# Kernel tuning notes

Measured on AMD Instinct MI355X. Metric: run time of the kernel, lower is better.

Reference implementation:

```python
import jax, jax.numpy as jnp
import numpy as np
import math

MAX_T = 1000

def _timestep_emb(t, emb_dim):
    half = emb_dim // 2
    freqs = jnp.exp(jnp.arange(half, dtype=jnp.float32) * -(math.log(MAX_T) / (half - 1)))
    e = t.astype(jnp.float32)[:, None] * freqs[None, :]
    return jnp.concatenate([jnp.sin(e), jnp.cos(e)], axis=1)  # [bs, emb_dim]


def setup_inputs() -> dict:
    key = jax.random.key(0)
    ks = jax.random.split(key, 12)
    BS, N, D, H = 16, 1024, 128, 8  # batch, nodes(=in_channels), out_dim(=d), heads
    w = lambda k, shape: jax.random.normal(k, shape, dtype=jnp.float32) * 0.05
    return {
        "A_t": jax.random.normal(ks[0], (BS, N, N), dtype=jnp.float32),
        "F_c": jax.random.normal(ks[1], (BS, N, D), dtype=jnp.float32),
        "t": jax.random.randint(ks[2], (BS,), 0, MAX_T),
        "Wq": w(ks[3], (D, D * H)), "bq": jnp.zeros((D * H,), jnp.float32),
        "Wk": w(ks[4], (D, D * H)), "bk": jnp.zeros((D * H,), jnp.float32),
        "Wv": w(ks[5], (D, D * H)), "bv": jnp.zeros((D * H,), jnp.float32),
        "Wo": w(ks[6], (D * H, D)), "bo": jnp.zeros((D,), jnp.float32),
        "Wg": jnp.eye(D, dtype=jnp.float32),  # GCN weight, eye init
    }


def reference(A_t, F_c, t, Wq, bq, Wk, bk, Wv, bv, Wo, bo, Wg):
    BS, N, D = F_c.shape
    H = Wq.shape[1] // D
    # timestep embedding, emb_dim = in_channels = N
    t_emb = _timestep_emb(t, N)                       # [bs, N]
    c = F_c + t_emb[:, :, None]                       # [bs, N, D]
    # naive multi-head self-attention with per-head dim = out_dim
    q = (c @ Wq + bq).reshape(BS, N, H, D).transpose(0, 2, 1, 3)
    k = (c @ Wk + bk).reshape(BS, N, H, D).transpose(0, 2, 1, 3)
    v = (c @ Wv + bv).reshape(BS, N, H, D).transpose(0, 2, 1, 3)
    scores = jnp.einsum('bhnd,bhmd->bhnm', q, k) / math.sqrt(D)
    a = jax.nn.softmax(scores, axis=-1)
    ctx = jnp.einsum('bhnm,bhmd->bhnd', a, v)
    ctx = ctx.transpose(0, 2, 1, 3).reshape(BS, N, H * D)
    h = ctx @ Wo + bo                                 # [bs, N, D]
    # GCN: relu(A @ (h @ W))
    feat = jax.nn.relu(A_t @ (h @ Wg))                # [bs, N, D]
    # Corr: row-normalize (unbiased std, matching torch.std) then bmm
    mu = feat.mean(axis=-1, keepdims=True)
    std = jnp.std(feat, axis=-1, ddof=1, keepdims=True)
    norm = (feat - mu) / (std + 1e-8)
    return jnp.einsum('bnd,bmd->bnm', norm, norm) / feat.shape[-1]
```

## Files before the change

### kernel.cpp

```cpp
#include <hip/hip_runtime.h>
#include <math.h>

#define NN 1024
#define DD 128
#define HH 8

typedef __attribute__((ext_vector_type(8))) short short8;
typedef __attribute__((ext_vector_type(4))) float f32x4;

__device__ inline unsigned short f2bf(float x) {
    union { float f; unsigned u; } v; v.f = x;
    return (unsigned short)((v.u + 0x7FFF + ((v.u >> 16) & 1)) >> 16);
}
__device__ inline unsigned pack2(float a, float b) {
    return (unsigned)f2bf(a) | ((unsigned)f2bf(b) << 16);
}

__global__ __launch_bounds__(256) void k_prep_w(
    const float* __restrict__ Wq, const float* __restrict__ Wk, const float* __restrict__ Wv,
    const float* __restrict__ Wo, const float* __restrict__ Wg,
    unsigned short* WqT, unsigned short* WkT, unsigned short* WvT,
    unsigned short* WoT, unsigned short* WgT) {
    int id = blockIdx.x;
    const float* src; unsigned short* dst; int R, C, ti;
    if (id < 128)      { src = Wq; dst = WqT; R = 128;  C = 1024; ti = id; }
    else if (id < 256) { src = Wk; dst = WkT; R = 128;  C = 1024; ti = id - 128; }
    else if (id < 384) { src = Wv; dst = WvT; R = 128;  C = 1024; ti = id - 256; }
    else if (id < 512) { src = Wo; dst = WoT; R = 1024; C = 128;  ti = id - 384; }
    else               { src = Wg; dst = WgT; R = 128;  C = 128;  ti = id - 512; }
    int tc = C >> 5;
    int r0 = (ti / tc) << 5, c0 = (ti % tc) << 5;
    __shared__ float T[32][33];
    int tid = threadIdx.x;
    int r = tid >> 3, c4 = (tid & 7) << 2;
    float4 v = *(const float4*)&src[(size_t)(r0 + r) * C + c0 + c4];
    T[r][c4] = v.x; T[r][c4 + 1] = v.y; T[r][c4 + 2] = v.z; T[r][c4 + 3] = v.w;
    __syncthreads();
    int c = tid >> 3, r4 = (tid & 7) << 2;
    uint2 o;
    o.x = pack2(T[r4][c], T[r4 + 1][c]);
    o.y = pack2(T[r4 + 2][c], T[r4 + 3][c]);
    *(uint2*)&dst[(size_t)(c0 + c) * R + r0 + r4] = o;
}

__global__ __launch_bounds__(256) void k_embed(const float* __restrict__ F_c,
                                               const int* __restrict__ t,
                                               unsigned short* __restrict__ cb) {
    int gi = blockIdx.x * 256 + threadIdx.x;
    int row = gi >> 4, ch = gi & 15;
    int b = row >> 10, n = row & 1023;
    float tv = (float)t[b];
    int j = n & 511;
    float e = tv * expf(-(float)j * 0.013518112092919054f);
    float emb = (n < 512) ? sinf(e) : cosf(e);
    const float* src = F_c + (size_t)row * 128 + ch * 8;
    float4 a = *(const float4*)src;
    float4 c4 = *(const float4*)(src + 4);
    uint4 o;
    o.x = pack2(a.x + emb, a.y + emb);  o.y = pack2(a.z + emb, a.w + emb);
    o.z = pack2(c4.x + emb, c4.y + emb); o.w = pack2(c4.z + emb, c4.w + emb);
    *(uint4*)&cb[(size_t)row * 128 + ch * 8] = o;
}

__global__ __launch_bounds__(256) void k_proj(const unsigned short* __restrict__ Ain,
                                              const unsigned short* __restrict__ WT,
                                              const float* __restrict__ bias,
                                              unsigned short* __restrict__ Out,
                                              float scale, int mode, int bh_mul) {
    __shared__ __align__(16) unsigned short sm[2 * 128 * 136];
    unsigned short* CT  = sm;
    unsigned short* WTs = sm + 128 * 136;
    int tid = threadIdx.x;
    int m0 = blockIdx.x * 128;
    int head = blockIdx.y;
    int w = tid >> 6, lane = tid & 63, n16 = lane & 15, quad = lane >> 4;
#pragma unroll
    for (int p = 0; p < 8; ++p) {
        int idx = tid + p * 256;
        int r = idx >> 4, ch = idx & 15;
        *(uint4*)&CT[r * 136 + ch * 8]  = *(const uint4*)&Ain[(size_t)(m0 + r) * 128 + ch * 8];
        *(uint4*)&WTs[r * 136 + ch * 8] = *(const uint4*)&WT[(size_t)(head * 128 + r) * 128 + ch * 8];
    }
    __syncthreads();
    int wr = (w >> 1) * 64, wc = (w & 1) * 64;
    f32x4 acc[4][4];
#pragma unroll
    for (int i = 0; i < 4; i++)
#pragma unroll
        for (int j = 0; j < 4; j++) acc[i][j] = (f32x4){0.f, 0.f, 0.f, 0.f};
#pragma unroll
    for (int kk = 0; kk < 4; ++kk) {
        short8 af[4], bf[4];
#pragma unroll
        for (int rb = 0; rb < 4; ++rb)
            af[rb] = *(const short8*)&CT[(wr + rb * 16 + n16) * 136 + kk * 32 + quad * 8];
#pragma unroll
        for (int cb = 0; cb < 4; ++cb)
            bf[cb] = *(const short8*)&WTs[(wc + cb * 16 + n16) * 136 + kk * 32 + quad * 8];
#pragma unroll
        for (int rb = 0; rb < 4; ++rb)
#pragma unroll
            for (int cb = 0; cb < 4; ++cb)
                acc[rb][cb] = __builtin_amdgcn_mfma_f32_16x16x32_bf16(af[rb], bf[cb], acc[rb][cb], 0, 0, 0);
    }
    __syncthreads();
#pragma unroll
    for (int rb = 0; rb < 4; ++rb)
#pragma unroll
        for (int cb = 0; cb < 4; ++cb) {
            int colb = wc + cb * 16 + n16;
            float bs = bias ? bias[head * 128 + colb] : 0.f;
#pragma unroll
            for (int reg = 0; reg < 4; ++reg) {
                int rowb = wr + rb * 16 + quad * 4 + reg;
                unsigned short val = f2bf((acc[rb][cb][reg] + bs) * scale);
                if (mode == 0) CT[rowb * 136 + colb] = val;
                else           CT[colb * 136 + rowb] = val;
            }
        }
    __syncthreads();
    int b = m0 >> 10, n0 = m0 & 1023;
    size_t base = (size_t)(b * bh_mul + head) * 131072;
    if (mode == 0) {
#pragma unroll
        for (int p = 0; p < 8; ++p) {
            int idx = tid + p * 256;
            int r = idx >> 4, ch = idx & 15;
            *(uint4*)&Out[base + (size_t)(n0 + r) * 128 + ch * 8] = *(const uint4*)&CT[r * 136 + ch * 8];
        }
    } else {
#pragma unroll
        for (int p = 0; p < 8; ++p) {
            int idx = tid + p * 256;
            int r = idx >> 4, ch = idx & 15;
            *(uint4*)&Out[base + (size_t)r * 1024 + n0 + ch * 8] = *(const uint4*)&CT[r * 136 + ch * 8];
        }
    }
}

__global__ __launch_bounds__(256, 2) void k_attn2(const unsigned short* __restrict__ qbuf,
                                                  const unsigned short* __restrict__ kbuf,
                                                  const unsigned short* __restrict__ vtb,
                                                  unsigned short* __restrict__ ctxb) {
    __shared__ __align__(16) unsigned short sm[17920];
    unsigned short* Ks = sm;
    unsigned short* Vt = sm + 8704;

    const int tid = threadIdx.x;
    const int w = tid >> 6, lane = tid & 63;
    const int n16 = lane & 15, quad = lane >> 4;
    const int g = blockIdx.x;
    const int bh = g & 127, tileq = g >> 7;

    const unsigned short* Qp = qbuf + (size_t)bh * 131072 + (size_t)tileq * 16384;
    const unsigned short* Kp = kbuf + (size_t)bh * 131072;
    const unsigned short* Vp = vtb + (size_t)bh * 131072;

    short8 qf[2][4];
#pragma unroll
    for (int qb2 = 0; qb2 < 2; ++qb2)
#pragma unroll
        for (int dc = 0; dc < 4; ++dc)
            qf[qb2][dc] = *(const short8*)&Qp[(size_t)(w * 32 + qb2 * 16 + n16) * 128 + dc * 32 + quad * 8];

    float mrun[2] = {-1e30f, -1e30f};
    float lrun[2] = {0.f, 0.f};
    f32x4 O[2][8];
#pragma unroll
    for (int qb2 = 0; qb2 < 2; ++qb2)
#pragma unroll
        for (int dc = 0; dc < 8; ++dc) O[qb2][dc] = (f32x4){0.f, 0.f, 0.f, 0.f};

    const int vr0 = tid >> 3;
    const int k0 = (tid & 7) * 8;
    const int slotA = ((k0 >> 5) << 5) | (((k0 >> 2) & 3) << 3) | (((k0 >> 4) & 1) << 2);

    uint4 kreg[4], vreg[4];
#pragma unroll
    for (int p = 0; p < 4; ++p) {
        int idx = tid + p * 256;
        int r = idx >> 4, ch = idx & 15;
        kreg[p] = *(const uint4*)&Kp[(size_t)r * 128 + ch * 8];
        vreg[p] = *(const uint4*)&Vp[(size_t)(vr0 + p * 32) * 1024 + k0];
    }

    for (int kt = 0; kt < 16; ++kt) {
#pragma unroll
        for (int p = 0; p < 4; ++p) {
            int idx = tid + p * 256;
            int r = idx >> 4, ch = idx & 15;
            *(uint4*)&Ks[r * 136 + ch * 8] = kreg[p];
        }
#pragma unroll
        for (int p = 0; p < 4; ++p) {
            int r = vr0 + p * 32;
            *(uint2*)&Vt[r * 72 + slotA]     = make_uint2(vreg[p].x, vreg[p].y);
            *(uint2*)&Vt[r * 72 + slotA + 8] = make_uint2(vreg[p].z, vreg[p].w);
        }
        __syncthreads();

        if (kt < 15) {
#pragma unroll
            for (int p = 0; p < 4; ++p) {
                int idx = tid + p * 256;
                int r = idx >> 4, ch = idx & 15;
                kreg[p] = *(const uint4*)&Kp[(size_t)((kt + 1) * 64 + r) * 128 + ch * 8];
                vreg[p] = *(const uint4*)&Vp[(size_t)(vr0 + p * 32) * 1024 + (kt + 1) * 64 + k0];
            }
        }

        f32x4 S[2][4];
#pragma unroll
        for (int qb2 = 0; qb2 < 2; ++qb2)
#pragma unroll
            for (int kb = 0; kb < 4; ++kb) S[qb2][kb] = (f32x4){0.f, 0.f, 0.f, 0.f};
        __builtin_amdgcn_s_setprio(1);
#pragma unroll
        for (int kb = 0; kb < 4; ++kb)
#pragma unroll
            for (int dc = 0; dc < 4; ++dc) {
                short8 kf = *(const short8*)&Ks[(kb * 16 + n16) * 136 + dc * 32 + quad * 8];
                S[0][kb] = __builtin_amdgcn_mfma_f32_16x16x32_bf16(kf, qf[0][dc], S[0][kb], 0, 0, 0);
                S[1][kb] = __builtin_amdgcn_mfma_f32_16x16x32_bf16(kf, qf[1][dc], S[1][kb], 0, 0, 0);
            }
        __builtin_amdgcn_s_setprio(0);

        float mx[2];
#pragma unroll
        for (int qb2 = 0; qb2 < 2; ++qb2) {
            float m = S[qb2][0][0];
#pragma unroll
            for (int kb = 0; kb < 4; ++kb)
#pragma unroll
                for (int reg = 0; reg < 4; ++reg) m = fmaxf(m, S[qb2][kb][reg]);
            m = fmaxf(m, __shfl_xor(m, 16));
            m = fmaxf(m, __shfl_xor(m, 32));
            mx[qb2] = m;
        }
        int keep = (mx[0] - mrun[0] <= 1.f) && (mx[1] - mrun[1] <= 1.f);
        if (!__all(keep)) {
            float mn0 = fmaxf(mrun[0], mx[0]);
            float mn1 = fmaxf(mrun[1], mx[1]);
            float a0 = __expf(mrun[0] - mn0);
            float a1 = __expf(mrun[1] - mn1);
            mrun[0] = mn0; mrun[1] = mn1;
            lrun[0] *= a0; lrun[1] *= a1;
            float av0[4], av1[4];
#pragma unroll
            for (int reg = 0; reg < 4; ++reg) {
                av0[reg] = __shfl(a0, quad * 4 + reg);
                av1[reg] = __shfl(a1, quad * 4 + reg);
            }
#pragma unroll
            for (int dc = 0; dc < 8; ++dc)
#pragma unroll
                for (int reg = 0; reg < 4; ++reg) {
                    O[0][dc][reg] *= av0[reg];
                    O[1][dc][reg] *= av1[reg];
                }
        }
#pragma unroll
        for (int qb2 = 0; qb2 < 2; ++qb2) {
            float ps = 0.f;
#pragma unroll
            for (int kb = 0; kb < 4; ++kb)
#pragma unroll
                for (int reg = 0; reg < 4; ++reg) {
                    float p = __expf(S[qb2][kb][reg] - mrun[qb2]);
                    S[qb2][kb][reg] = p;
                    ps += p;
                }
            ps += __shfl_xor(ps, 16);
            ps += __shfl_xor(ps, 32);
            lrun[qb2] += ps;
        }
        unsigned pk01[2][4], pk23[2][4];
#pragma unroll
        for (int qb2 = 0; qb2 < 2; ++qb2)
#pragma unroll
            for (int kb = 0; kb < 4; ++kb) {
                asm("v_cvt_pk_bf16_f32 %0, %1, %2"
                    : "=v"(pk01[qb2][kb]) : "v"(S[qb2][kb][0]), "v"(S[qb2][kb][1]));
                asm("v_cvt_pk_bf16_f32 %0, %1, %2"
                    : "=v"(pk23[qb2][kb]) : "v"(S[qb2][kb][2]), "v"(S[qb2][kb][3]));
            }
        __builtin_amdgcn_s_setprio(1);
#pragma unroll
        for (int c = 0; c < 2; ++c) {
            union { uint4 u; short8 s; } pa0, pa1;
            pa0.u = make_uint4(pk01[0][2 * c], pk23[0][2 * c], pk01[0][2 * c + 1], pk23[0][2 * c + 1]);
            pa1.u = make_uint4(pk01[1][2 * c], pk23[1][2 * c], pk01[1][2 * c + 1], pk23[1][2 * c + 1]);
#pragma unroll
            for (int dc = 0; dc < 8; ++dc) {
                short8 vf = *(const short8*)&Vt[(dc * 16 + n16) * 72 + c * 32 + quad * 8];
                O[0][dc] = __builtin_amdgcn_mfma_f32_16x16x32_bf16(pa0.s, vf, O[0][dc], 0, 0, 0);
                O[1][dc] = __builtin_amdgcn_mfma_f32_16x16x32_bf16(pa1.s, vf, O[1][dc], 0, 0, 0);
            }
        }
        __builtin_amdgcn_s_setprio(0);
        __syncthreads();
    }

    float lv[2][4];
#pragma unroll
    for (int qb2 = 0; qb2 < 2; ++qb2)
#pragma unroll
        for (int reg = 0; reg < 4; ++reg)
            lv[qb2][reg] = 1.f / __shfl(lrun[qb2], quad * 4 + reg);
    unsigned short* Ct = sm;
#pragma unroll
    for (int qb2 = 0; qb2 < 2; ++qb2)
#pragma unroll
        for (int reg = 0; reg < 4; ++reg) {
            int row = w * 32 + qb2 * 16 + quad * 4 + reg;
#pragma unroll
            for (int dc = 0; dc < 8; ++dc)
                Ct[row * 136 + dc * 16 + n16] = f2bf(O[qb2][dc][reg] * lv[qb2][reg]);
        }
    __syncthreads();
    unsigned short* Outp = ctxb + (size_t)bh * 131072 + (size_t)tileq * 16384;
#pragma unroll
    for (int p = 0; p < 8; ++p) {
        int idx = tid + p * 256;
        int r = idx >> 4, ch = idx & 15;
        *(uint4*)&Outp[(size_t)r * 128 + ch * 8] = *(const uint4*)&Ct[r * 136 + ch * 8];
    }
}

__global__ __launch_bounds__(256) void k_proj_o(const unsigned short* __restrict__ Ctxb,
                                                const unsigned short* __restrict__ WoT,
                                                const float* __restrict__ bo,
                                                unsigned short* __restrict__ Hb) {
    __shared__ __align__(16) unsigned short sm[64 * 72 + 128 * 72];
    unsigned short* As = sm;
    unsigned short* Bs = sm + 64 * 72;
    int tid = threadIdx.x;
    int m0 = blockIdx.x * 64;
    int b = m0 >> 10, n0 = m0 & 1023;
    int w = tid >> 6, lane = tid & 63, n16 = lane & 15, quad = lane >> 4;
    int wr = (w & 1) * 32, wc = (w >> 1) * 64;
    f32x4 acc[2][4];
#pragma unroll
    for (int i = 0; i < 2; i++)
#pragma unroll
        for (int j = 0; j < 4; j++) acc[i][j] = (f32x4){0.f, 0.f, 0.f, 0.f};
    for (int kt = 0; kt < 16; ++kt) {
        __syncthreads();
        int hh = kt >> 1, d0 = (kt & 1) * 64;
#pragma unroll
        for (int p = 0; p < 2; ++p) {
            int idx = tid + p * 256;
            int r = idx >> 3, ch = idx & 7;
            *(uint4*)&As[r * 72 + ch * 8] =
                *(const uint4*)&Ctxb[((size_t)(b * 8 + hh) * 1024 + n0 + r) * 128 + d0 + ch * 8];
        }
#pragma unroll
        for (int p = 0; p < 4; ++p) {
            int idx = tid + p * 256;
            int r = idx >> 3, ch = idx & 7;
            *(uint4*)&Bs[r * 72 + ch * 8] = *(const uint4*)&WoT[(size_t)r * 1024 + kt * 64 + ch * 8];
        }
        __syncthreads();
#pragma unroll
        for (int kk = 0; kk < 2; ++kk) {
            short8 af0 = *(const short8*)&As[(wr + n16) * 72 + kk * 32 + quad * 8];
            short8 af1 = *(const short8*)&As[(wr + 16 + n16) * 72 + kk * 32 + quad * 8];
#pragma unroll
            for (int cb = 0; cb < 4; ++cb) {
                short8 bf = *(const short8*)&Bs[(wc + cb * 16 + n16) * 72 + kk * 32 + quad * 8];
                acc[0][cb] = __builtin_amdgcn_mfma_f32_16x16x32_bf16(af0, bf, acc[0][cb], 0, 0, 0);
                acc[1][cb] = __builtin_amdgcn_mfma_f32_16x16x32_bf16(af1, bf, acc[1][cb], 0, 0, 0);
            }
        }
    }
    __syncthreads();
    unsigned short* Ct = sm;
#pragma unroll
    for (int rb = 0; rb < 2; ++rb)
#pragma unroll
        for (int cb = 0; cb < 4; ++cb) {
            int col = wc + cb * 16 + n16;
            float bs = bo[col];
#pragma unroll
            for (int reg = 0; reg < 4; ++reg)
                Ct[(wr + rb * 16 + quad * 4 + reg) * 136 + col] = f2bf(acc[rb][cb][reg] + bs);
        }
    __syncthreads();
#pragma unroll
    for (int p = 0; p < 4; ++p) {
        int idx = tid + p * 256;
        int r = idx >> 4, ch = idx & 15;
        *(uint4*)&Hb[(size_t)(m0 + r) * 128 + ch * 8] = *(const uint4*)&Ct[r * 136 + ch * 8];
    }
}

__global__ __launch_bounds__(256) void k_at_gemm(const float* __restrict__ At,
                                                 const unsigned short* __restrict__ HgT,
                                                 float* __restrict__ Feat) {
    __shared__ __align__(16) unsigned short sm[64 * 72 + 128 * 72];
    unsigned short* As = sm;
    unsigned short* Bs = sm + 64 * 72;
    int tid = threadIdx.x;
    int bz = blockIdx.z;
    int m0 = blockIdx.x * 64;
    int w = tid >> 6, lane = tid & 63, n16 = lane & 15, quad = lane >> 4;
    int wr = (w & 1) * 32, wc = (w >> 1) * 64;
    f32x4 acc[2][4];
#pragma unroll
    for (int i = 0; i < 2; i++)
#pragma unroll
        for (int j = 0; j < 4; j++) acc[i][j] = (f32x4){0.f, 0.f, 0.f, 0.f};
    for (int kt = 0; kt < 16; ++kt) {
        __syncthreads();
#pragma unroll
        for (int p = 0; p < 2; ++p) {
            int idx = tid + p * 256;
            int r = idx >> 3, ch = idx & 7;
            const float* s = At + (size_t)bz * 1048576 + (size_t)(m0 + r) * 1024 + kt * 64 + ch * 8;
            float4 x = *(const float4*)s;
            float4 y = *(const float4*)(s + 4);
            uint4 o;
            o.x = pack2(x.x, x.y); o.y = pack2(x.z, x.w);
            o.z = pack2(y.x, y.y); o.w = pack2(y.z, y.w);
            *(uint4*)&As[r * 72 + ch * 8] = o;
        }
#pragma unroll
        for (int p = 0; p < 4; ++p) {
            int idx = tid + p * 256;
            int r = idx >> 3, ch = idx & 7;
            *(uint4*)&Bs[r * 72 + ch * 8] =
                *(const uint4*)&HgT[(size_t)bz * 131072 + (size_t)r * 1024 + kt * 64 + ch * 8];
        }
        __syncthreads();
#pragma unroll
        for (int kk = 0; kk < 2; ++kk) {
            short8 af0 = *(const short8*)&As[(wr + n16) * 72 + kk * 32 + quad * 8];
            short8 af1 = *(const short8*)&As[(wr + 16 + n16) * 72 + kk * 32 + quad * 8];
#pragma unroll
            for (int cb = 0; cb < 4; ++cb) {
                short8 bf = *(const short8*)&Bs[(wc + cb * 16 + n16) * 72 + kk * 32 + quad * 8];
                acc[0][cb] = __builtin_amdgcn_mfma_f32_16x16x32_bf16(af0, bf, acc[0][cb], 0, 0, 0);
                acc[1][cb] = __builtin_amdgcn_mfma_f32_16x16x32_bf16(af1, bf, acc[1][cb], 0, 0, 0);
            }
        }
    }
#pragma unroll
    for (int rb = 0; rb < 2; ++rb)
#pragma unroll
        for (int cb = 0; cb < 4; ++cb) {
            int col = wc + cb * 16 + n16;
#pragma unroll
            for (int reg = 0; reg < 4; ++reg) {
                int row = m0 + wr + rb * 16 + quad * 4 + reg;
                Feat[(size_t)bz * 131072 + (size_t)row * 128 + col] = fmaxf(acc[rb][cb][reg], 0.f);
            }
        }
}

__global__ __launch_bounds__(64) void k_norm(const float* __restrict__ F,
                                             unsigned short* __restrict__ Nb) {
    int row = blockIdx.x, tdx = threadIdx.x;
    const float* p = F + (size_t)row * 128;
    float2 xy = *(const float2*)&p[tdx * 2];
    float sum = xy.x + xy.y;
#pragma unroll
    for (int off = 32; off; off >>= 1) sum += __shfl_xor(sum, off);
    float mu = sum * (1.f / 128.f);
    float d0 = xy.x - mu, d1 = xy.y - mu;
    float sq = d0 * d0 + d1 * d1;
#pragma unroll
    for (int off = 32; off; off >>= 1) sq += __shfl_xor(sq, off);
    float sd = sqrtf(sq * (1.f / 127.f));
    float inv = 1.f / (sd + 1e-8f);
    ((unsigned*)Nb)[(size_t)row * 64 + tdx] = pack2(d0 * inv, d1 * inv);
}

__global__ __launch_bounds__(256) void k_corr(const unsigned short* __restrict__ Nb,
                                              float* __restrict__ Out) {
    __shared__ __align__(16) unsigned short sm[2 * 128 * 136];
    unsigned short* Ar = sm;
    unsigned short* Br = sm + 128 * 136;
    int tid = threadIdx.x;
    int bz = blockIdx.z;
    int n0 = blockIdx.x * 128, m0 = blockIdx.y * 128;
    const unsigned short* base = Nb + (size_t)bz * 131072;
    int w = tid >> 6, lane = tid & 63, n16 = lane & 15, quad = lane >> 4;
#pragma unroll
    for (int p = 0; p < 8; ++p) {
        int idx = tid + p * 256;
        int r = idx >> 4, ch = idx & 15;
        *(uint4*)&Ar[r * 136 + ch * 8] = *(const uint4*)&base[(size_t)(n0 + r) * 128 + ch * 8];
        *(uint4*)&Br[r * 136 + ch * 8] = *(const uint4*)&base[(size_t)(m0 + r) * 128 + ch * 8];
    }
    __syncthreads();
    int wr = (w >> 1) * 64, wc = (w & 1) * 64;
    f32x4 acc[4][4];
#pragma unroll
    for (int i = 0; i < 4; i++)
#pragma unroll
        for (int j = 0; j < 4; j++) acc[i][j] = (f32x4){0.f, 0.f, 0.f, 0.f};
#pragma unroll
    for (int kk = 0; kk < 4; ++kk) {
        short8 af[4], bf[4];
#pragma unroll
        for (int rb = 0; rb < 4; ++rb)
            af[rb] = *(const short8*)&Ar[(wr + rb * 16 + n16) * 136 + kk * 32 + quad * 8];
#pragma unroll
        for (int cb = 0; cb < 4; ++cb)
            bf[cb] = *(const short8*)&Br[(wc + cb * 16 + n16) * 136 + kk * 32 + quad * 8];
#pragma unroll
        for (int rb = 0; rb < 4; ++rb)
#pragma unroll
            for (int cb = 0; cb < 4; ++cb)
                acc[rb][cb] = __builtin_amdgcn_mfma_f32_16x16x32_bf16(af[rb], bf[cb], acc[rb][cb], 0, 0, 0);
    }
#pragma unroll
    for (int rb = 0; rb < 4; ++rb)
#pragma unroll
        for (int cb = 0; cb < 4; ++cb)
#pragma unroll
            for (int reg = 0; reg < 4; ++reg) {
                int row = n0 + wr + rb * 16 + quad * 4 + reg;
                int col = m0 + wc + cb * 16 + n16;
                Out[(size_t)bz * 1048576 + (size_t)row * 1024 + col] = acc[rb][cb][reg] * 0.0078125f;
            }
}

extern "C" void kernel_launch(void* const* d_in, const int* in_sizes, int n_in,
                              void* d_out, int out_size, void* d_ws, size_t ws_size,
                              hipStream_t stream) {
    const float* A_t = (const float*)d_in[0];
    const float* F_c = (const float*)d_in[1];
    const int*   t   = (const int*)d_in[2];
    const float* Wq  = (const float*)d_in[3];
    const float* bq  = (const float*)d_in[4];
    const float* Wk  = (const float*)d_in[5];
    const float* bk  = (const float*)d_in[6];
    const float* Wv  = (const float*)d_in[7];
    const float* bv  = (const float*)d_in[8];
    const float* Wo  = (const float*)d_in[9];
    const float* bo  = (const float*)d_in[10];
    const float* Wg  = (const float*)d_in[11];
    float* out = (float*)d_out;
    char* ws = (char*)d_ws;

    unsigned short* cb   = (unsigned short*)(ws);
    unsigned short* qb   = (unsigned short*)(ws + 4194304);
    unsigned short* kbuf = (unsigned short*)(ws + 37748736);
    unsigned short* vtb  = (unsigned short*)(ws + 71303168);
    unsigned short* ctxb = (unsigned short*)(ws + 104857600);
    unsigned short* hb   = (unsigned short*)(ws + 138412032);
    unsigned short* hgT  = (unsigned short*)(ws + 142606336);
    float*          feat = (float*)        (ws + 146800640);
    unsigned short* nb   = (unsigned short*)(ws + 155189248);
    unsigned short* WqT  = (unsigned short*)(ws + 159383552);
    unsigned short* WkT  = (unsigned short*)(ws + 159645696);
    unsigned short* WvT  = (unsigned short*)(ws + 159907840);
    unsigned short* WoT  = (unsigned short*)(ws + 160169984);
    unsigned short* WgT  = (unsigned short*)(ws + 160432128);

    const float qscale = 0.08838834764831845f;

    k_prep_w<<<528, 256, 0, stream>>>(Wq, Wk, Wv, Wo, Wg, WqT, WkT, WvT, WoT, WgT);
    k_embed<<<1024, 256, 0, stream>>>(F_c, t, cb);
    k_proj<<<dim3(128, 8), 256, 0, stream>>>(cb, WqT, bq, qb,   qscale, 0, 8);
    k_proj<<<dim3(128, 8), 256, 0, stream>>>(cb, WkT, bk, kbuf, 1.f,    0, 8);
    k_proj<<<dim3(128, 8), 256, 0, stream>>>(cb, WvT, bv, vtb,  1.f,    1, 8);
    k_attn2<<<1024, 256, 0, stream>>>(qb, kbuf, vtb, ctxb);
    k_proj_o<<<256, 256, 0, stream>>>(ctxb, WoT, bo, hb);
    k_proj<<<dim3(128, 1), 256, 0, stream>>>(hb, WgT, nullptr, hgT, 1.f, 1, 1);
    k_at_gemm<<<dim3(16, 1, 16), 256, 0, stream>>>(A_t, hgT, feat);
    k_norm<<<16384, 64, 0, stream>>>(feat, nb);
    k_corr<<<dim3(8, 8, 16), 256, 0, stream>>>(nb, out);
}
```

Measured before the change: 396.4 us.

## Double-buffer K/V tiles in attention and merge QKV projections into one launch

The attention kernel now keeps two shared-memory buffers for K and V tiles and prefetches two tiles ahead into registers. The next tile is written to the alternate buffer while the current one is computed, which drops one barrier per iteration. Separately, the three Q/K/V projection launches are merged into one grid using a z dimension, saving launch overhead and giving a larger grid. In exchange, attention shared memory doubles to about 70KB per block and register pressure rises from the extra prefetch buffers, which may hurt the two-blocks-per-CU occupancy target.

New measurement: 404.6 us. 1.02x slower.

```diff
diff --git a/kernel.cpp b/kernel.cpp
--- a/kernel.cpp
+++ b/kernel.cpp
@@ -62,90 +62,253 @@
     *(uint4*)&cb[(size_t)row * 128 + ch * 8] = o;
 }
 
+__device__ __forceinline__ void proj_body(const unsigned short* __restrict__ Ain,
+                                          const unsigned short* __restrict__ WT,
+                                          const float* __restrict__ bias,
+                                          unsigned short* __restrict__ Out,
+                                          float scale, int mode, int bh_mul,
+                                          unsigned short* sm, int head, int m0) {
+    unsigned short* CT  = sm;
+    unsigned short* WTs = sm + 128 * 136;
+    int tid = threadIdx.x;
+    int w = tid >> 6, lane = tid & 63, n16 = lane & 15, quad = lane >> 4;
+#pragma unroll
+    for (int p = 0; p < 8; ++p) {
+        int idx = tid + p * 256;
+        int r = idx >> 4, ch = idx & 15;
+        *(uint4*)&CT[r * 136 + ch * 8]  = *(const uint4*)&Ain[(size_t)(m0 + r) * 128 + ch * 8];
+        *(uint4*)&WTs[r * 136 + ch * 8] = *(const uint4*)&WT[(size_t)(head * 128 + r) * 128 + ch * 8];
+    }
+    __syncthreads();
+    int wr = (w >> 1) * 64, wc = (w & 1) * 64;
+    f32x4 acc[4][4];
+#pragma unroll
+    for (int i = 0; i < 4; i++)
+#pragma unroll
+        for (int j = 0; j < 4; j++) acc[i][j] = (f32x4){0.f, 0.f, 0.f, 0.f};
+#pragma unroll
+    for (int kk = 0; kk < 4; ++kk) {
+        short8 af[4], bf[4];
+#pragma unroll
+        for (int rb = 0; rb < 4; ++rb)
+            af[rb] = *(const short8*)&CT[(wr + rb * 16 + n16) * 136 + kk * 32 + quad * 8];
+#pragma unroll
+        for (int cb = 0; cb < 4; ++cb)
+            bf[cb] = *(const short8*)&WTs[(wc + cb * 16 + n16) * 136 + kk * 32 + quad * 8];
+#pragma unroll
+        for (int rb = 0; rb < 4; ++rb)
+#pragma unroll
+            for (int cb = 0; cb < 4; ++cb)
+                acc[rb][cb] = __builtin_amdgcn_mfma_f32_16x16x32_bf16(af[rb], bf[cb], acc[rb][cb], 0, 0, 0);
+    }
+    __syncthreads();
+#pragma unroll
+    for (int rb = 0; rb < 4; ++rb)
+#pragma unroll
+        for (int cb = 0; cb < 4; ++cb) {
+            int colb = wc + cb * 16 + n16;
+            float bs = bias ? bias[head * 128 + colb] : 0.f;
+#pragma unroll
+            for (int reg = 0; reg < 4; ++reg) {
+                int rowb = wr + rb * 16 + quad * 4 + reg;
+                unsigned short val = f2bf((acc[rb][cb][reg] + bs) * scale);
+                if (mode == 0) CT[rowb * 136 + colb] = val;
+                else           CT[colb * 136 + rowb] = val;
+            }
+        }
+    __syncthreads();
+    int b = m0 >> 10, n0 = m0 & 1023;
+    size_t base = (size_t)(b * bh_mul + head) * 131072;
+    if (mode == 0) {
+#pragma unroll
+        for (int p = 0; p < 8; ++p) {
+            int idx = tid + p * 256;
+            int r = idx >> 4, ch = idx & 15;
+            *(uint4*)&Out[base + (size_t)(n0 + r) * 128 + ch * 8] = *(const uint4*)&CT[r * 136 + ch * 8];
+        }
+    } else {
+#pragma unroll
+        for (int p = 0; p < 8; ++p) {
+            int idx = tid + p * 256;
+            int r = idx >> 4, ch = idx & 15;
+            *(uint4*)&Out[base + (size_t)r * 1024 + n0 + ch * 8] = *(const uint4*)&CT[r * 136 + ch * 8];
+        }
+    }
+}
+
+__global__ __launch_bounds__(256) void k_proj_qkv(const unsigned short* __restrict__ Ain,
+                                                  const unsigned short* __restrict__ W0,
+                                                  const unsigned short* __restrict__ W1,
+                                                  const unsigned short* __restrict__ W2,
+                                                  const float* __restrict__ b0,
+                                                  const float* __restrict__ b1,
+                                                  const float* __restrict__ b2,
+                                                  unsigned short* __restrict__ O0,
+                                                  unsigned short* __restrict__ O1,
+                                                  unsigned short* __restrict__ O2,
+                                                  float qscale) {
+    __shared__ __align__(16) unsigned short sm[2 * 128 * 136];
+    int z = blockIdx.z;
+    const unsigned short* WT = (z == 0) ? W0 : (z == 1) ? W1 : W2;
+    const float* bias = (z == 0) ? b0 : (z == 1) ? b1 : b2;
+    unsigned short* Out = (z == 0) ? O0 : (z == 1) ? O1 : O2;
+    float scale = (z == 0) ? qscale : 1.f;
+    int mode = (z == 2) ? 1 : 0;
+    proj_body(Ain, WT, bias, Out, scale, mode, 8, sm, blockIdx.y, blockIdx.x * 128);
+}
+
 __global__ __launch_bounds__(256) void k_proj(const unsigned short* __restrict__ Ain,
                                               const unsigned short* __restrict__ WT,
                                               const float* __restrict__ bias,
                                               unsigned short* __restrict__ Out,
                                               float scale, int mode, int bh_mul) {
     __shared__ __align__(16) unsigned short sm[2 * 128 * 136];
-    unsigned short* CT  = sm;
-    unsigned short* WTs = sm + 128 * 136;
-    int tid = threadIdx.x;
-    int m0 = blockIdx.x * 128;
-    int head = blockIdx.y;
-    int w = tid >> 6, lane = tid & 63, n16 = lane & 15, quad = lane >> 4;
-#pragma unroll
-    for (int p = 0; p < 8; ++p) {
-        int idx = tid + p * 256;
-        int r = idx >> 4, ch = idx & 15;
-        *(uint4*)&CT[r * 136 + ch * 8]  = *(const uint4*)&Ain[(size_t)(m0 + r) * 128 + ch * 8];
-        *(uint4*)&WTs[r * 136 + ch * 8] = *(const uint4*)&WT[(size_t)(head * 128 + r) * 128 + ch * 8];
-    }
-    __syncthreads();
-    int wr = (w >> 1) * 64, wc = (w & 1) * 64;
-    f32x4 acc[4][4];
-#pragma unroll
-    for (int i = 0; i < 4; i++)
-#pragma unroll
-        for (int j = 0; j < 4; j++) acc[i][j] = (f32x4){0.f, 0.f, 0.f, 0.f};
-#pragma unroll
-    for (int kk = 0; kk < 4; ++kk) {
-        short8 af[4], bf[4];
-#pragma unroll
-        for (int rb = 0; rb < 4; ++rb)
-            af[rb] = *(const short8*)&CT[(wr + rb * 16 + n16) * 136 + kk * 32 + quad * 8];
-#pragma unroll
-        for (int cb = 0; cb < 4; ++cb)
-            bf[cb] = *(const short8*)&WTs[(wc + cb * 16 + n16) * 136 + kk * 32 + quad * 8];
-#pragma unroll
-        for (int rb = 0; rb < 4; ++rb)
-#pragma unroll
-            for (int cb = 0; cb < 4; ++cb)
-                acc[rb][cb] = __builtin_amdgcn_mfma_f32_16x16x32_bf16(af[rb], bf[cb], acc[rb][cb], 0, 0, 0);
-    }
-    __syncthreads();
-#pragma unroll
-    for (int rb = 0; rb < 4; ++rb)
-#pragma unroll
-        for (int cb = 0; cb < 4; ++cb) {
-            int colb = wc + cb * 16 + n16;
-            float bs = bias ? bias[head * 128 + colb] : 0.f;
+    proj_body(Ain, WT, bias, Out, scale, mode, bh_mul, sm, blockIdx.y, blockIdx.x * 128);
+}
+
+__device__ __forceinline__ void attn_compute(const unsigned short* __restrict__ Ksc,
+                                             const unsigned short* __restrict__ Vtc,
+                                             const short8 (&qf)[2][4],
+                                             float (&mrun)[2], float (&lrun)[2],
+                                             f32x4 (&O)[2][8], int n16, int quad) {
+    f32x4 S[2][4];
+#pragma unroll
+    for (int qb2 = 0; qb2 < 2; ++qb2)
+#pragma unroll
+        for (int kb = 0; kb < 4; ++kb) S[qb2][kb] = (f32x4){0.f, 0.f, 0.f, 0.f};
+    __builtin_amdgcn_s_setprio(1);
+#pragma unroll
+    for (int kb = 0; kb < 4; ++kb)
+#pragma unroll
+        for (int dc = 0; dc < 4; ++dc) {
+            short8 kf = *(const short8*)&Ksc[(kb * 16 + n16) * 136 + dc * 32 + quad * 8];
+            S[0][kb] = __builtin_amdgcn_mfma_f32_16x16x32_bf16(kf, qf[0][dc], S[0][kb], 0, 0, 0);
+            S[1][kb] = __builtin_amdgcn_mfma_f32_16x16x32_bf16(kf, qf[1][dc], S[1][kb], 0, 0, 0);
+        }
+    __builtin_amdgcn_s_setprio(0);
+
+    float mx[2];
+#pragma unroll
+    for (int qb2 = 0; qb2 < 2; ++qb2) {
+        float m = S[qb2][0][0];
+#pragma unroll
+        for (int kb = 0; kb < 4; ++kb)
+#pragma unroll
+            for (int reg = 0; reg < 4; ++reg) m = fmaxf(m, S[qb2][kb][reg]);
+        m = fmaxf(m, __shfl_xor(m, 16));
+        m = fmaxf(m, __shfl_xor(m, 32));
+        mx[qb2] = m;
+    }
+    int keep = (mx[0] - mrun[0] <= 1.f) && (mx[1] - mrun[1] <= 1.f);
+    if (!__all(keep)) {
+        float mn0 = fmaxf(mrun[0], mx[0]);
+        float mn1 = fmaxf(mrun[1], mx[1]);
+        float a0 = __expf(mrun[0] - mn0);
+        float a1 = __expf(mrun[1] - mn1);
+        mrun[0] = mn0; mrun[1] = mn1;
+        lrun[0] *= a0; lrun[1] *= a1;
+        float av0[4], av1[4];
+#pragma unroll
+        for (int reg = 0; reg < 4; ++reg) {
+            av0[reg] = __shfl(a0, quad * 4 + reg);
+            av1[reg] = __shfl(a1, quad * 4 + reg);
+        }
+#pragma unroll
+        for (int dc = 0; dc < 8; ++dc)
 #pragma unroll
             for (int reg = 0; reg < 4; ++reg) {
-                int rowb = wr + rb * 16 + quad * 4 + reg;
-                unsigned short val = f2bf((acc[rb][cb][reg] + bs) * scale);
-                if (mode == 0) CT[rowb * 136 + colb] = val;
-                else           CT[colb * 136 + rowb] = val;
+                O[0][dc][reg] *= av0[reg];
+                O[1][dc][reg] *= av1[reg];
             }
-        }
-    __syncthreads();
-    int b = m0 >> 10, n0 = m0 & 1023;
-    size_t base = (size_t)(b * bh_mul + head) * 131072;
-    if (mode == 0) {
-#pragma unroll
-        for (int p = 0; p < 8; ++p) {
+    }
+#pragma unroll
+    for (int qb2 = 0; qb2 < 2; ++qb2) {
+        float ps = 0.f;
+#pragma unroll
+        for (int kb = 0; kb < 4; ++kb)
+#pragma unroll
+            for (int reg = 0; reg < 4; ++reg) {
+                float p = __expf(S[qb2][kb][reg] - mrun[qb2]);
+                S[qb2][kb][reg] = p;
+                ps += p;
+            }
+        ps += __shfl_xor(ps, 16);
+        ps += __shfl_xor(ps, 32);
+        lrun[qb2] += ps;
+    }
+    unsigned pk01[2][4], pk23[2][4];
+#pragma unroll
+    for (int qb2 = 0; qb2 < 2; ++qb2)
+#pragma unroll
+        for (int kb = 0; kb < 4; ++kb) {
+            asm("v_cvt_pk_bf16_f32 %0, %1, %2"
+                : "=v"(pk01[qb2][kb]) : "v"(S[qb2][kb][0]), "v"(S[qb2][kb][1]));
+            asm("v_cvt_pk_bf16_f32 %0, %1, %2"
+                : "=v"(pk23[qb2][kb]) : "v"(S[qb2][kb][2]), "v"(S[qb2][kb][3]));
+        }
+    __builtin_amdgcn_s_setprio(1);
+#pragma unroll
+    for (int c = 0; c < 2; ++c) {
+        union { uint4 u; short8 s; } pa0, pa1;
+        pa0.u = make_uint4(pk01[0][2 * c], pk23[0][2 * c], pk01[0][2 * c + 1], pk23[0][2 * c + 1]);
+        pa1.u = make_uint4(pk01[1][2 * c], pk23[1][2 * c], pk01[1][2 * c + 1], pk23[1][2 * c + 1]);
+#pragma unroll
+        for (int dc = 0; dc < 8; ++dc) {
+            short8 vf = *(const short8*)&Vtc[(dc * 16 + n16) * 72 + c * 32 + quad * 8];
+            O[0][dc] = __builtin_amdgcn_mfma_f32_16x16x32_bf16(pa0.s, vf, O[0][dc], 0, 0, 0);
+            O[1][dc] = __builtin_amdgcn_mfma_f32_16x16x32_bf16(pa1.s, vf, O[1][dc], 0, 0, 0);
+        }
+    }
+    __builtin_amdgcn_s_setprio(0);
+}
+
+__device__ __forceinline__ void attn_step(int kt,
+                                          const unsigned short* __restrict__ Kp,
+                                          const unsigned short* __restrict__ Vp,
+                                          unsigned short* sm, int tid, int vr0, int k0, int slotA,
+                                          uint4 (&LK)[4], uint4 (&LV)[4],
+                                          uint4 (&WK)[4], uint4 (&WV)[4],
+                                          const short8 (&qf)[2][4],
+                                          float (&mrun)[2], float (&lrun)[2],
+                                          f32x4 (&O)[2][8], int n16, int quad) {
+    if (kt + 2 < 16) {
+#pragma unroll
+        for (int p = 0; p < 4; ++p) {
             int idx = tid + p * 256;
             int r = idx >> 4, ch = idx & 15;
-            *(uint4*)&Out[base + (size_t)(n0 + r) * 128 + ch * 8] = *(const uint4*)&CT[r * 136 + ch * 8];
-        }
-    } else {
-#pragma unroll
-        for (int p = 0; p < 8; ++p) {
+            LK[p] = *(const uint4*)&Kp[(size_t)((kt + 2) * 64 + r) * 128 + ch * 8];
+            LV[p] = *(const uint4*)&Vp[(size_t)(vr0 + p * 32) * 1024 + (kt + 2) * 64 + k0];
+        }
+    }
+    if (kt + 1 < 16) {
+        unsigned short* Kw = sm + ((kt + 1) & 1) * 17920;
+        unsigned short* Vw = Kw + 8704;
+#pragma unroll
+        for (int p = 0; p < 4; ++p) {
             int idx = tid + p * 256;
             int r = idx >> 4, ch = idx & 15;
-            *(uint4*)&Out[base + (size_t)r * 1024 + n0 + ch * 8] = *(const uint4*)&CT[r * 136 + ch * 8];
-        }
-    }
+            *(uint4*)&Kw[r * 136 + ch * 8] = WK[p];
+        }
+#pragma unroll
+        for (int p = 0; p < 4; ++p) {
+            int r = vr0 + p * 32;
+            *(uint2*)&Vw[r * 72 + slotA]     = make_uint2(WV[p].x, WV[p].y);
+            *(uint2*)&Vw[r * 72 + slotA + 8] = make_uint2(WV[p].z, WV[p].w);
+        }
+    }
+    {
+        const unsigned short* Ksc = sm + (kt & 1) * 17920;
+        const unsigned short* Vtc = Ksc + 8704;
+        attn_compute(Ksc, Vtc, qf, mrun, lrun, O, n16, quad);
+    }
+    __syncthreads();
 }
 
 __global__ __launch_bounds__(256, 2) void k_attn2(const unsigned short* __restrict__ qbuf,
                                                   const unsigned short* __restrict__ kbuf,
                                                   const unsigned short* __restrict__ vtb,
                                                   unsigned short* __restrict__ ctxb) {
-    __shared__ __align__(16) unsigned short sm[17920];
-    unsigned short* Ks = sm;
-    unsigned short* Vt = sm + 8704;
-
+    __shared__ __align__(16) unsigned short sm[35840];
     const int tid = threadIdx.x;
     const int w = tid >> 6, lane = tid & 63;
     const int n16 = lane & 15, quad = lane >> 4;
@@ -175,130 +338,40 @@
     const int k0 = (tid & 7) * 8;
     const int slotA = ((k0 >> 5) << 5) | (((k0 >> 2) & 3) << 3) | (((k0 >> 4) & 1) << 2);
 
-    uint4 kreg[4], vreg[4];
+    uint4 ka[4], va[4], kb4[4], vb4[4];
 #pragma unroll
     for (int p = 0; p < 4; ++p) {
         int idx = tid + p * 256;
         int r = idx >> 4, ch = idx & 15;
-        kreg[p] = *(const uint4*)&Kp[(size_t)r * 128 + ch * 8];
-        vreg[p] = *(const uint4*)&Vp[(size_t)(vr0 + p * 32) * 1024 + k0];
-    }
-
-    for (int kt = 0; kt < 16; ++kt) {
+        ka[p]  = *(const uint4*)&Kp[(size_t)r * 128 + ch * 8];
+        va[p]  = *(const uint4*)&Vp[(size_t)(vr0 + p * 32) * 1024 + k0];
+        kb4[p] = *(const uint4*)&Kp[(size_t)(64 + r) * 128 + ch * 8];
+        vb4[p] = *(const uint4*)&Vp[(size_t)(vr0 + p * 32) * 1024 + 64 + k0];
+    }
+    {
+        unsigned short* Kw = sm;
+        unsigned short* Vw = sm + 8704;
 #pragma unroll
         for (int p = 0; p < 4; ++p) {
             int idx = tid + p * 256;
             int r = idx >> 4, ch = idx & 15;
-            *(uint4*)&Ks[r * 136 + ch * 8] = kreg[p];
+            *(uint4*)&Kw[r * 136 + ch * 8] = ka[p];
         }
 #pragma unroll
         for (int p = 0; p < 4; ++p) {
             int r = vr0 + p * 32;
-            *(uint2*)&Vt[r * 72 + slotA]     = make_uint2(vreg[p].x, vreg[p].y);
-            *(uint2*)&Vt[r * 72 + slotA + 8] = make_uint2(vreg[p].z, vreg[p].w);
-        }
-        __syncthreads();
-
-        if (kt < 15) {
-#pragma unroll
-            for (int p = 0; p < 4; ++p) {
-                int idx = tid + p * 256;
-                int r = idx >> 4, ch = idx & 15;
-                kreg[p] = *(const uint4*)&Kp[(size_t)((kt + 1) * 64 + r) * 128 + ch * 8];
-                vreg[p] = *(const uint4*)&Vp[(size_t)(vr0 + p * 32) * 1024 + (kt + 1) * 64 + k0];
-            }
-        }
-
-        f32x4 S[2][4];
-#pragma unroll
-        for (int qb2 = 0; qb2 < 2; ++qb2)
-#pragma unroll
-            for (int kb = 0; kb < 4; ++kb) S[qb2][kb] = (f32x4){0.f, 0.f, 0.f, 0.f};
-        __builtin_amdgcn_s_setprio(1);
-#pragma unroll
-        for (int kb = 0; kb < 4; ++kb)
-#pragma unroll
-            for (int dc = 0; dc < 4; ++dc) {
-                short8 kf = *(const short8*)&Ks[(kb * 16 + n16) * 136 + dc * 32 + quad * 8];
-                S[0][kb] = __builtin_amdgcn_mfma_f32_16x16x32_bf16(kf, qf[0][dc], S[0][kb], 0, 0, 0);
-                S[1][kb] = __builtin_amdgcn_mfma_f32_16x16x32_bf16(kf, qf[1][dc], S[1][kb], 0, 0, 0);
-            }
-        __builtin_amdgcn_s_setprio(0);
-
-        float mx[2];
-#pragma unroll
-        for (int qb2 = 0; qb2 < 2; ++qb2) {
-            float m = S[qb2][0][0];
-#pragma unroll
-            for (int kb = 0; kb < 4; ++kb)
-#pragma unroll
-                for (int reg = 0; reg < 4; ++reg) m = fmaxf(m, S[qb2][kb][reg]);
-            m = fmaxf(m, __shfl_xor(m, 16));
-            m = fmaxf(m, __shfl_xor(m, 32));
-            mx[qb2] = m;
-        }
-        int keep = (mx[0] - mrun[0] <= 1.f) && (mx[1] - mrun[1] <= 1.f);
-        if (!__all(keep)) {
-            float mn0 = fmaxf(mrun[0], mx[0]);
-            float mn1 = fmaxf(mrun[1], mx[1]);
-            float a0 = __expf(mrun[0] - mn0);
-            float a1 = __expf(mrun[1] - mn1);
-            mrun[0] = mn0; mrun[1] = mn1;
-            lrun[0] *= a0; lrun[1] *= a1;
-            float av0[4], av1[4];
-#pragma unroll
-            for (int reg = 0; reg < 4; ++reg) {
-                av0[reg] = __shfl(a0, quad * 4 + reg);
-                av1[reg] = __shfl(a1, quad * 4 + reg);
-            }
-#pragma unroll
-            for (int dc = 0; dc < 8; ++dc)
-#pragma unroll
-                for (int reg = 0; reg < 4; ++reg) {
-                    O[0][dc][reg] *= av0[reg];
-                    O[1][dc][reg] *= av1[reg];
-                }
-        }
-#pragma unroll
-        for (int qb2 = 0; qb2 < 2; ++qb2) {
-            float ps = 0.f;
-#pragma unroll
-            for (int kb = 0; kb < 4; ++kb)
-#pragma unroll
-                for (int reg = 0; reg < 4; ++reg) {
-                    float p = __expf(S[qb2][kb][reg] - mrun[qb2]);
-                    S[qb2][kb][reg] = p;
-                    ps += p;
-                }
-            ps += __shfl_xor(ps, 16);
-            ps += __shfl_xor(ps, 32);
-            lrun[qb2] += ps;
-        }
-        unsigned pk01[2][4], pk23[2][4];
-#pragma unroll
-        for (int qb2 = 0; qb2 < 2; ++qb2)
-#pragma unroll
-            for (int kb = 0; kb < 4; ++kb) {
-                asm("v_cvt_pk_bf16_f32 %0, %1, %2"
-                    : "=v"(pk01[qb2][kb]) : "v"(S[qb2][kb][0]), "v"(S[qb2][kb][1]));
-                asm("v_cvt_pk_bf16_f32 %0, %1, %2"
-                    : "=v"(pk23[qb2][kb]) : "v"(S[qb2][kb][2]), "v"(S[qb2][kb][3]));
-            }
-        __builtin_amdgcn_s_setprio(1);
-#pragma unroll
-        for (int c = 0; c < 2; ++c) {
-            union { uint4 u; short8 s; } pa0, pa1;
-            pa0.u = make_uint4(pk01[0][2 * c], pk23[0][2 * c], pk01[0][2 * c + 1], pk23[0][2 * c + 1]);
-            pa1.u = make_uint4(pk01[1][2 * c], pk23[1][2 * c], pk01[1][2 * c + 1], pk23[1][2 * c + 1]);
-#pragma unroll
-            for (int dc = 0; dc < 8; ++dc) {
-                short8 vf = *(const short8*)&Vt[(dc * 16 + n16) * 72 + c * 32 + quad * 8];
-                O[0][dc] = __builtin_amdgcn_mfma_f32_16x16x32_bf16(pa0.s, vf, O[0][dc], 0, 0, 0);
-                O[1][dc] = __builtin_amdgcn_mfma_f32_16x16x32_bf16(pa1.s, vf, O[1][dc], 0, 0, 0);
-            }
-        }
-        __builtin_amdgcn_s_setprio(0);
-        __syncthreads();
+            *(uint2*)&Vw[r * 72 + slotA]     = make_uint2(va[p].x, va[p].y);
+            *(uint2*)&Vw[r * 72 + slotA + 8] = make_uint2(va[p].z, va[p].w);
+        }
+    }
+    __syncthreads();
+
+    for (int t = 0; t < 8; ++t) {
+        int kt0 = 2 * t, kt1 = 2 * t + 1;
+        attn_step(kt0, Kp, Vp, sm, tid, vr0, k0, slotA, ka, va, kb4, vb4,
+                  qf, mrun, lrun, O, n16, quad);
+        attn_step(kt1, Kp, Vp, sm, tid, vr0, k0, slotA, kb4, vb4, ka, va,
+                  qf, mrun, lrun, O, n16, quad);
     }
 
     float lv[2][4];
@@ -563,9 +636,8 @@
 
     k_prep_w<<<528, 256, 0, stream>>>(Wq, Wk, Wv, Wo, Wg, WqT, WkT, WvT, WoT, WgT);
     k_embed<<<1024, 256, 0, stream>>>(F_c, t, cb);
-    k_proj<<<dim3(128, 8), 256, 0, stream>>>(cb, WqT, bq, qb,   qscale, 0, 8);
-    k_proj<<<dim3(128, 8), 256, 0, stream>>>(cb, WkT, bk, kbuf, 1.f,    0, 8);
-    k_proj<<<dim3(128, 8), 256, 0, stream>>>(cb, WvT, bv, vtb,  1.f,    1, 8);
+    k_proj_qkv<<<dim3(128, 8, 3), 256, 0, stream>>>(cb, WqT, WkT, WvT, bq, bk, bv,
+                                                    qb, kbuf, vtb, qscale);
     k_attn2<<<1024, 256, 0, stream>>>(qb, kbuf, vtb, ctxb);
     k_proj_o<<<256, 256, 0, stream>>>(ctxb, WoT, bo, hb);
     k_proj<<<dim3(128, 1), 256, 0, stream>>>(hb, WgT, nullptr, hgT, 1.f, 1, 1);
```
